# Kernel optimization log

Measured on AMD Instinct MI355X. Metric: run time of the kernel, lower is better.

The kernel has to match this reference:

```python
import jax, jax.numpy as jnp
import numpy as np

N = 100000
E = 3200000
C = 40
L_CORR = 10
L_SMOOTH = 10
ALPHA_CORR = 0.979
ALPHA_SMOOTH = 0.756


def setup_inputs() -> dict:
    key = jax.random.key(0)
    k1, k2, k3, k4 = jax.random.split(key, 4)
    y_true = jax.random.randint(k1, (N,), 0, C, dtype=jnp.int32)
    y_soft = jax.random.uniform(k2, (N, C), dtype=jnp.float32)
    y_soft = y_soft / y_soft.sum(axis=1, keepdims=True)
    spread_mask = jax.random.randint(k3, (N,), 0, 2, dtype=jnp.int32).astype(bool)
    edge_index = jax.random.randint(k4, (2, E), 0, N, dtype=jnp.int32)
    return {"y_true": y_true, "y_soft": y_soft, "spread_mask": spread_mask,
            "edge_index": edge_index}


def _gcn_norm(src, dst, n):
    # symmetric normalization D^-1/2 A D^-1/2 from the edge list
    deg = jax.ops.segment_sum(jnp.ones_like(dst, dtype=jnp.float32), dst,
                              num_segments=n)
    dinv = jnp.where(deg > 0, jax.lax.rsqrt(jnp.maximum(deg, 1.0)), 0.0)
    return dinv[src] * dinv[dst]  # [E]


def _label_prop(y0, src, dst, norm, n, alpha, n_layers, post_step):
    # out <- post_step(alpha * A_hat @ out + (1 - alpha) * y0), repeated
    def body(_, out):
        agg = jax.ops.segment_sum(out[src] * norm[:, None], dst,
                                  num_segments=n)  # [N, C]
        return post_step(alpha * agg + (1.0 - alpha) * y0)
    return jax.lax.fori_loop(0, n_layers, body, y0)


def _correct_and_smooth(y_true, y_soft, spread_mask, edge_index):
    src, dst = edge_index[0], edge_index[1]
    norm = _gcn_norm(src, dst, N)
    onehot = jax.nn.one_hot(y_true, C, dtype=y_soft.dtype)  # [N, C]
    m = spread_mask[:, None]

    # ---- correct: propagate masked residual error, autoscale path ----
    error = jnp.where(m, onehot - y_soft, 0.0)
    smoothed_error = _label_prop(error, src, dst, norm, N, ALPHA_CORR,
                                 L_CORR, lambda x: jnp.clip(x, -1.0, 1.0))
    numel = jnp.sum(spread_mask).astype(y_soft.dtype)
    sigma = jnp.sum(jnp.abs(error)) / numel  # error is zero off-mask
    denom = jnp.sum(jnp.abs(smoothed_error), axis=1, keepdims=True)
    scale = sigma / denom  # [N, 1]
    scale = jnp.where(jnp.isinf(scale) | (scale > 1000.0), 1.0, scale)
    y_corr = y_soft + scale * smoothed_error

    # ---- smooth: inject true labels on spread_mask, propagate w/ softmax ----
    y0 = jnp.where(m, onehot, y_corr)
    out = _label_prop(y0, src, dst, norm, N, ALPHA_SMOOTH, L_SMOOTH,
                      lambda x: jax.nn.softmax(x, axis=-1))
    return out


def reference(y_true, y_soft, spread_mask, edge_index):
    return _correct_and_smooth(y_true, y_soft, spread_mask, edge_index)
```

## Files before the change

kernel.cpp:

```cpp
#include <hip/hip_runtime.h>
#include <hip/hip_fp16.h>
#include <math.h>

#define C 40

__global__ void k_detect(const unsigned int* __restrict__ w, int nwords,
                         unsigned int* __restrict__ flags) {
    int i = blockIdx.x * blockDim.x + threadIdx.x;
    unsigned int viol = 0;
    for (; i < nwords; i += gridDim.x * blockDim.x) {
        unsigned int v = w[i];
        if (!(v == 0u || v == 1u)) viol |= 1u;
        if (!(v == 0u || v == 0x3F800000u)) viol |= 2u;
    }
    if (viol) atomicOr(flags, viol);
}

__device__ __forceinline__ bool read_mask(const void* mp, unsigned int fl, int n) {
    if ((fl & 1u) == 0u) return ((const int*)mp)[n] != 0;
    if ((fl & 2u) == 0u) return ((const float*)mp)[n] != 0.0f;
    return ((const unsigned char*)mp)[n] != 0;
}

__global__ void k_slot(const int* __restrict__ dst, int* __restrict__ fill,
                       int* __restrict__ slots, int E) {
    int e = blockIdx.x * blockDim.x + threadIdx.x;
    if (e < E) slots[e] = atomicAdd(&fill[dst[e]], 1);
}

__global__ void k_dinv(const int* __restrict__ deg, float* __restrict__ dinv, int n) {
    int i = blockIdx.x * blockDim.x + threadIdx.x;
    if (i < n) {
        int d = deg[i];
        dinv[i] = (d > 0) ? rsqrtf((float)d) : 0.0f;
    }
}

__global__ void k_scan1(const int* __restrict__ in, int* __restrict__ outp,
                        int* __restrict__ bsum, int n) {
    __shared__ int sm[256];
    int tid = threadIdx.x;
    int i = blockIdx.x * 256 + tid;
    int v = (i < n) ? in[i] : 0;
    sm[tid] = v;
    __syncthreads();
#pragma unroll
    for (int o = 1; o < 256; o <<= 1) {
        int t = (tid >= o) ? sm[tid - o] : 0;
        __syncthreads();
        sm[tid] += t;
        __syncthreads();
    }
    if (i <= n) outp[i] = sm[tid] - v;
    if (tid == 255) bsum[blockIdx.x] = sm[255];
}

__global__ void k_scan2(int* __restrict__ bsum, int nb) {
    __shared__ int sm[512];
    int tid = threadIdx.x;
    int v = (tid < nb) ? bsum[tid] : 0;
    sm[tid] = v;
    __syncthreads();
    for (int o = 1; o < 512; o <<= 1) {
        int t = (tid >= o) ? sm[tid - o] : 0;
        __syncthreads();
        sm[tid] += t;
        __syncthreads();
    }
    if (tid < nb) bsum[tid] = sm[tid] - v;
}

__global__ void k_scan3(int* __restrict__ outp, const int* __restrict__ bsum, int n) {
    int i = blockIdx.x * 256 + threadIdx.x;
    if (i <= n) outp[i] += bsum[blockIdx.x];
}

__global__ void k_wr(const int* __restrict__ src, const int* __restrict__ dst,
                     const int* __restrict__ slots, const float* __restrict__ dinv,
                     const int* __restrict__ rowptr,
                     unsigned long long* __restrict__ pk, int E) {
    int e = blockIdx.x * blockDim.x + threadIdx.x;
    if (e < E) {
        int d = dst[e], s = src[e];
        int pos = rowptr[d] + slots[e];
        unsigned long long u = (unsigned)s |
            ((unsigned long long)(unsigned)__float_as_int(dinv[s] * dinv[d]) << 32);
        pk[pos] = u;
    }
}

__global__ __launch_bounds__(256) void k_error(
    const float4* __restrict__ ys4, const int* __restrict__ y_true,
    const void* __restrict__ maskp, const unsigned int* __restrict__ flags,
    char* __restrict__ err, float* __restrict__ psig, float* __restrict__ pcnt,
    int n) {
    unsigned int fl = *flags;
    unsigned boff = (unsigned)n * 64u;
    float a = 0.f, cnt = 0.f;
    int nq = n * 10;
    for (int i = blockIdx.x * blockDim.x + threadIdx.x; i < nq;
         i += gridDim.x * blockDim.x) {
        int node = i / 10;
        int q = i - node * 10;
        float e0 = 0.f, e1 = 0.f, e2 = 0.f, e3 = 0.f;
        if (read_mask(maskp, fl, node)) {
            int yt = y_true[node];
            float4 ys = ys4[i];
            int c0 = q * 4;
            e0 = ((c0 + 0) == yt ? 1.f : 0.f) - ys.x;
            e1 = ((c0 + 1) == yt ? 1.f : 0.f) - ys.y;
            e2 = ((c0 + 2) == yt ? 1.f : 0.f) - ys.z;
            e3 = ((c0 + 3) == yt ? 1.f : 0.f) - ys.w;
            a += fabsf(e0) + fabsf(e1) + fabsf(e2) + fabsf(e3);
            if (q == 0) cnt += 1.f;
        }
        __half2 h01 = __floats2half2_rn(e0, e1);
        __half2 h23 = __floats2half2_rn(e2, e3);
        uint2 w;
        w.x = *(unsigned*)&h01;
        w.y = *(unsigned*)&h23;
        unsigned off = (q < 8) ? (unsigned)node * 64u + (unsigned)q * 8u
                               : boff + (unsigned)node * 16u + (unsigned)(q - 8) * 8u;
        *(uint2*)(err + off) = w;
    }
    __shared__ float sA[256];
    __shared__ float sB[256];
    int tid = threadIdx.x;
    sA[tid] = a; sB[tid] = cnt;
    __syncthreads();
    for (int o = 128; o; o >>= 1) {
        if (tid < o) { sA[tid] += sA[tid + o]; sB[tid] += sB[tid + o]; }
        __syncthreads();
    }
    if (tid == 0) { psig[blockIdx.x] = sA[0]; pcnt[blockIdx.x] = sB[0]; }
}

__global__ __launch_bounds__(256) void k_reduce(
    const float* __restrict__ psig, const float* __restrict__ pcnt,
    float* __restrict__ s_sig, float* __restrict__ s_cnt, int nb) {
    float a = 0.f, c = 0.f;
    for (int i = threadIdx.x; i < nb; i += 256) { a += psig[i]; c += pcnt[i]; }
    __shared__ float sA[256];
    __shared__ float sB[256];
    int tid = threadIdx.x;
    sA[tid] = a; sB[tid] = c;
    __syncthreads();
    for (int o = 128; o; o >>= 1) {
        if (tid < o) { sA[tid] += sA[tid + o]; sB[tid] += sB[tid + o]; }
        __syncthreads();
    }
    if (tid == 0) { *s_sig = sA[0]; *s_cnt = sB[0]; }
}

template <int POST, int F32OUT>
__global__ __launch_bounds__(256, 2) void k_prop(
    const int* __restrict__ rowptr, const unsigned long long* __restrict__ pk8,
    const char* __restrict__ xc, const char* __restrict__ y0,
    void* __restrict__ outv, float alpha, float beta, int n) {
    int wid = (blockIdx.x * blockDim.x + threadIdx.x) >> 6;
    int lane = threadIdx.x & 63;
    if (wid >= n) return;
    int beg = __builtin_amdgcn_readfirstlane(rowptr[wid]);
    int end = __builtin_amdgcn_readfirstlane(rowptr[wid + 1]);
    int deg = end - beg;
    int j = lane / 10;
    int k = lane - j * 10;
    unsigned shift = (k < 8) ? 6u : 4u;
    unsigned off = (k < 8) ? (unsigned)(k * 8)
                           : (unsigned)n * 64u + (unsigned)((k - 8) * 8);

    uint2 yv = *(const uint2*)(y0 + (((unsigned)wid << shift) + off));
    __half2 yh01 = *(__half2*)&yv.x;
    __half2 yh23 = *(__half2*)&yv.y;
    float2 yf01 = __half22float2(yh01);
    float2 yf23 = __half22float2(yh23);

    float a0 = 0.f, a1 = 0.f, a2 = 0.f, a3 = 0.f;

    unsigned s_[8];
    float n_[8];
    int dm1 = (deg > 0) ? deg - 1 : 0;
#pragma unroll
    for (int i = 0; i < 8; ++i) {
        int idx = j + 6 * i;
        int cl = idx < dm1 ? idx : dm1;
        unsigned long long u = pk8[beg + cl];
        s_[i] = (unsigned)(u & 0xffffffffu);
        bool val = (lane < 60) && (idx < deg);
        n_[i] = val ? __int_as_float((int)(u >> 32)) : 0.0f;
    }
    uint2 xv[8];
#pragma unroll
    for (int i = 0; i < 8; ++i)
        xv[i] = *(const uint2*)(xc + (((unsigned)s_[i] << shift) + off));
#pragma unroll
    for (int i = 0; i < 8; ++i) {
        __half2 h01 = *(__half2*)&xv[i].x;
        __half2 h23 = *(__half2*)&xv[i].y;
        float2 f01 = __half22float2(h01);
        float2 f23 = __half22float2(h23);
        a0 = fmaf(n_[i], f01.x, a0); a1 = fmaf(n_[i], f01.y, a1);
        a2 = fmaf(n_[i], f23.x, a2); a3 = fmaf(n_[i], f23.y, a3);
    }

    int rem = deg - 48;
    if (rem > 0) {
        int jbig = (lane < 60) ? j : 0x40000000;
        unsigned jo = (unsigned)(((lane < 60) ? j : 5) * 8);
        const char* pkc = (const char*)(pk8 + beg);
        int t = 48;
        for (; rem > 0; rem -= 12, t += 12) {
            unsigned long long ua = *(const unsigned long long*)(pkc + (size_t)t * 8 + jo);
            unsigned long long ub = *(const unsigned long long*)(pkc + (size_t)(t + 6) * 8 + jo);
            unsigned sa = (unsigned)(ua & 0xffffffffu);
            unsigned sb = (unsigned)(ub & 0xffffffffu);
            uint2 xa = *(const uint2*)(xc + ((sa << shift) + off));
            uint2 xb = *(const uint2*)(xc + ((sb << shift) + off));
            float na = (jbig < rem) ? __int_as_float((int)(ua >> 32)) : 0.0f;
            float nb = (jbig < rem - 6) ? __int_as_float((int)(ub >> 32)) : 0.0f;
            __half2 ha01 = *(__half2*)&xa.x;
            __half2 ha23 = *(__half2*)&xa.y;
            float2 fa01 = __half22float2(ha01);
            float2 fa23 = __half22float2(ha23);
            a0 = fmaf(na, fa01.x, a0); a1 = fmaf(na, fa01.y, a1);
            a2 = fmaf(na, fa23.x, a2); a3 = fmaf(na, fa23.y, a3);
            __half2 hb01 = *(__half2*)&xb.x;
            __half2 hb23 = *(__half2*)&xb.y;
            float2 fb01 = __half22float2(hb01);
            float2 fb23 = __half22float2(hb23);
            a0 = fmaf(nb, fb01.x, a0); a1 = fmaf(nb, fb01.y, a1);
            a2 = fmaf(nb, fb23.x, a2); a3 = fmaf(nb, fb23.y, a3);
        }
    }

    a0 += __shfl(a0, lane + 30); a1 += __shfl(a1, lane + 30);
    a2 += __shfl(a2, lane + 30); a3 += __shfl(a3, lane + 30);
    float t0a = __shfl(a0, lane + 10), t1a = __shfl(a1, lane + 10);
    float t2a = __shfl(a2, lane + 10), t3a = __shfl(a3, lane + 10);
    float t0b = __shfl(a0, lane + 20), t1b = __shfl(a1, lane + 20);
    float t2b = __shfl(a2, lane + 20), t3b = __shfl(a3, lane + 20);
    a0 += t0a + t0b; a1 += t1a + t1b; a2 += t2a + t2b; a3 += t3a + t3b;

    float v0 = fmaf(alpha, a0, beta * yf01.x);
    float v1 = fmaf(alpha, a1, beta * yf01.y);
    float v2 = fmaf(alpha, a2, beta * yf23.x);
    float v3 = fmaf(alpha, a3, beta * yf23.y);

    bool valid = (lane < 10);
    float r0, r1, r2, r3;
    if (POST == 0) {
        r0 = fminf(1.0f, fmaxf(-1.0f, v0));
        r1 = fminf(1.0f, fmaxf(-1.0f, v1));
        r2 = fminf(1.0f, fmaxf(-1.0f, v2));
        r3 = fminf(1.0f, fmaxf(-1.0f, v3));
    } else {
        float mx = valid ? fmaxf(fmaxf(v0, v1), fmaxf(v2, v3)) : -3.0e38f;
#pragma unroll
        for (int o = 8; o; o >>= 1) mx = fmaxf(mx, __shfl_xor(mx, o));
        float e0 = valid ? __expf(v0 - mx) : 0.f;
        float e1 = valid ? __expf(v1 - mx) : 0.f;
        float e2 = valid ? __expf(v2 - mx) : 0.f;
        float e3 = valid ? __expf(v3 - mx) : 0.f;
        float ss = (e0 + e1) + (e2 + e3);
#pragma unroll
        for (int o = 8; o; o >>= 1) ss += __shfl_xor(ss, o);
        float inv = 1.0f / ss;
        r0 = e0 * inv; r1 = e1 * inv; r2 = e2 * inv; r3 = e3 * inv;
    }

    if (valid) {
        if (F32OUT) {
            ((float4*)outv)[(size_t)wid * 10 + k] = make_float4(r0, r1, r2, r3);
        } else {
            __half2 h01 = __floats2half2_rn(r0, r1);
            __half2 h23 = __floats2half2_rn(r2, r3);
            uint2 w;
            w.x = *(unsigned*)&h01;
            w.y = *(unsigned*)&h23;
            *(uint2*)((char*)outv + (((unsigned)wid << shift) + off)) = w;
        }
    }
}

__global__ __launch_bounds__(256) void k_scale(
    const char* __restrict__ sm_err, const float* __restrict__ y_soft,
    const int* __restrict__ y_true, const void* __restrict__ maskp,
    const unsigned int* __restrict__ flags, const float* __restrict__ s_sig,
    const float* __restrict__ s_cnt, char* __restrict__ y0, int n) {
    int wid = (blockIdx.x * blockDim.x + threadIdx.x) >> 6;
    int lane = threadIdx.x & 63;
    if (wid >= n) return;
    bool isA = (lane < 32);
    unsigned shift = isA ? 6u : 4u;
    unsigned aoff = isA ? (unsigned)(lane * 2)
                        : (unsigned)n * 64u + (unsigned)((lane - 32) * 2);
    float v = 0.f, a = 0.f;
    if (lane < C) {
        v = __half2float(*(const __half*)(sm_err + (((unsigned)wid << shift) + aoff)));
        a = fabsf(v);
    }
#pragma unroll
    for (int o = 32; o; o >>= 1) a += __shfl_xor(a, o);
    float sigma = (*s_sig) / (*s_cnt);
    float scale = sigma / a;
    if (isinf(scale) || scale > 1000.0f) scale = 1.0f;
    if (lane < C) {
        bool m = read_mask(maskp, *flags, wid);
        float yc = fmaf(scale, v, y_soft[(size_t)wid * C + lane]);
        float r = m ? ((lane == y_true[wid]) ? 1.0f : 0.0f) : yc;
        *(__half*)(y0 + (((unsigned)wid << shift) + aoff)) = __float2half(r);
    }
}

extern "C" void kernel_launch(void* const* d_in, const int* in_sizes, int n_in,
                              void* d_out, int out_size, void* d_ws, size_t ws_size,
                              hipStream_t stream) {
    const int* y_true = (const int*)d_in[0];
    const float* y_soft = (const float*)d_in[1];
    const void* maskp = d_in[2];
    const int* ei = (const int*)d_in[3];
    const int n = in_sizes[0];
    const int E = in_sizes[3] / 2;
    const int* src = ei;
    const int* dst = ei + E;

    char* ws = (char*)d_ws;
    size_t off = 0;
    auto alloc = [&](size_t bytes) -> char* {
        char* p = ws + off;
        off += (bytes + 255) & ~(size_t)255;
        return p;
    };
    int* fill = (int*)alloc((size_t)n * 4);
    unsigned int* flags = (unsigned int*)alloc(4);
    size_t zero_bytes = off;
    float* s_sig = (float*)alloc(4);
    float* s_cnt = (float*)alloc(4);
    float* psig = (float*)alloc(2048 * 4);
    float* pcnt = (float*)alloc(2048 * 4);
    float* dinv = (float*)alloc((size_t)n * 4);
    int* rowptr = (int*)alloc((size_t)(n + 1) * 4);
    int* bsum = (int*)alloc(4096);
    int* slots = (int*)alloc((size_t)E * 4);
    unsigned long long* pk = (unsigned long long*)alloc(((size_t)E + 64) * 8);
    size_t fb = (size_t)n * 80 + 512;
    char* hE = alloc(fb);
    char* hY = alloc(fb);
    char* hA = alloc(fb);
    char* hB = alloc(fb);
    (void)ws_size;

    hipMemsetAsync(d_ws, 0, zero_bytes, stream);
    hipMemsetAsync(pk + E, 0, 64 * 8, stream);

    k_detect<<<98, 256, 0, stream>>>((const unsigned int*)maskp, n / 4, flags);
    k_slot<<<(E + 255) / 256, 256, 0, stream>>>(dst, fill, slots, E);
    k_dinv<<<(n + 255) / 256, 256, 0, stream>>>(fill, dinv, n);

    int nb1 = (n + 1 + 255) / 256;
    k_scan1<<<nb1, 256, 0, stream>>>(fill, rowptr, bsum, n);
    k_scan2<<<1, 512, 0, stream>>>(bsum, nb1);
    k_scan3<<<nb1, 256, 0, stream>>>(rowptr, bsum, n);
    k_wr<<<(E + 255) / 256, 256, 0, stream>>>(src, dst, slots, dinv, rowptr, pk, E);

    k_error<<<2048, 256, 0, stream>>>((const float4*)y_soft, y_true, maskp, flags,
                                      hE, psig, pcnt, n);
    k_reduce<<<1, 256, 0, stream>>>(psig, pcnt, s_sig, s_cnt, 2048);

    const int pb = (n + 3) / 4;
    const float A1 = 0.979f, B1 = (float)(1.0 - 0.979);
    const float A2 = 0.756f, B2 = (float)(1.0 - 0.756);
    char* bufs[2] = { hA, hB };

    const char* x = hE;
    for (int it = 0; it < 10; ++it) {
        k_prop<0, 0><<<pb, 256, 0, stream>>>(rowptr, pk, x, hE, bufs[it & 1], A1, B1, n);
        x = bufs[it & 1];
    }
    k_scale<<<pb, 256, 0, stream>>>(x, y_soft, y_true, maskp, flags, s_sig, s_cnt, hY, n);

    x = hY;
    for (int it = 0; it < 9; ++it) {
        k_prop<1, 0><<<pb, 256, 0, stream>>>(rowptr, pk, x, hY, bufs[it & 1], A2, B2, n);
        x = bufs[it & 1];
    }
    k_prop<1, 1><<<pb, 256, 0, stream>>>(rowptr, pk, x, hY, d_out, A2, B2, n);
}
```

Baseline: 1.458 ms.

## Split propagation into two source-range passes to shrink gather working set

```diff
diff --git a/kernel.cpp b/kernel.cpp
--- a/kernel.cpp
+++ b/kernel.cpp
@@ -22,16 +22,20 @@
     return ((const unsigned char*)mp)[n] != 0;
 }
 
-__global__ void k_slot(const int* __restrict__ dst, int* __restrict__ fill,
-                       int* __restrict__ slots, int E) {
+__global__ void k_slot(const int* __restrict__ src, const int* __restrict__ dst,
+                       int* __restrict__ fill, int* __restrict__ slots,
+                       int E, int half, int n) {
     int e = blockIdx.x * blockDim.x + threadIdx.x;
-    if (e < E) slots[e] = atomicAdd(&fill[dst[e]], 1);
-}
-
-__global__ void k_dinv(const int* __restrict__ deg, float* __restrict__ dinv, int n) {
+    if (e < E) {
+        int h = (src[e] >= half) ? n : 0;
+        slots[e] = atomicAdd(&fill[h + dst[e]], 1);
+    }
+}
+
+__global__ void k_dinv(const int* __restrict__ fill, float* __restrict__ dinv, int n) {
     int i = blockIdx.x * blockDim.x + threadIdx.x;
     if (i < n) {
-        int d = deg[i];
+        int d = fill[i] + fill[n + i];
         dinv[i] = (d > 0) ? rsqrtf((float)d) : 0.0f;
     }
 }
@@ -58,16 +62,31 @@
 __global__ void k_scan2(int* __restrict__ bsum, int nb) {
     __shared__ int sm[512];
     int tid = threadIdx.x;
-    int v = (tid < nb) ? bsum[tid] : 0;
-    sm[tid] = v;
+    int K = (nb + 511) / 512;
+    if (K > 8) K = 8;
+    int base = tid * K;
+    int loc[8];
+    int s = 0;
+    for (int i = 0; i < K; ++i) {
+        int idx = base + i;
+        int v = (idx < nb) ? bsum[idx] : 0;
+        loc[i] = s;
+        s += v;
+    }
+    sm[tid] = s;
     __syncthreads();
+    int v = s;
     for (int o = 1; o < 512; o <<= 1) {
         int t = (tid >= o) ? sm[tid - o] : 0;
         __syncthreads();
         sm[tid] += t;
         __syncthreads();
     }
-    if (tid < nb) bsum[tid] = sm[tid] - v;
+    int pre = sm[tid] - v;
+    for (int i = 0; i < K; ++i) {
+        int idx = base + i;
+        if (idx < nb) bsum[idx] = pre + loc[i];
+    }
 }
 
 __global__ void k_scan3(int* __restrict__ outp, const int* __restrict__ bsum, int n) {
@@ -77,12 +96,13 @@
 
 __global__ void k_wr(const int* __restrict__ src, const int* __restrict__ dst,
                      const int* __restrict__ slots, const float* __restrict__ dinv,
-                     const int* __restrict__ rowptr,
-                     unsigned long long* __restrict__ pk, int E) {
+                     const int* __restrict__ rowptrAll,
+                     unsigned long long* __restrict__ pk, int E, int half, int n) {
     int e = blockIdx.x * blockDim.x + threadIdx.x;
     if (e < E) {
         int d = dst[e], s = src[e];
-        int pos = rowptr[d] + slots[e];
+        int h = (s >= half) ? n : 0;
+        int pos = rowptrAll[h + d] + slots[e];
         unsigned long long u = (unsigned)s |
             ((unsigned long long)(unsigned)__float_as_int(dinv[s] * dinv[d]) << 32);
         pk[pos] = u;
@@ -152,11 +172,12 @@
     if (tid == 0) { *s_sig = sA[0]; *s_cnt = sB[0]; }
 }
 
-template <int POST, int F32OUT>
+template <int POST, int F32OUT, int PASS>
 __global__ __launch_bounds__(256, 2) void k_prop(
     const int* __restrict__ rowptr, const unsigned long long* __restrict__ pk8,
     const char* __restrict__ xc, const char* __restrict__ y0,
-    void* __restrict__ outv, float alpha, float beta, int n) {
+    float4* __restrict__ tmp, void* __restrict__ outv,
+    float alpha, float beta, int n) {
     int wid = (blockIdx.x * blockDim.x + threadIdx.x) >> 6;
     int lane = threadIdx.x & 63;
     if (wid >= n) return;
@@ -169,32 +190,26 @@
     unsigned off = (k < 8) ? (unsigned)(k * 8)
                            : (unsigned)n * 64u + (unsigned)((k - 8) * 8);
 
-    uint2 yv = *(const uint2*)(y0 + (((unsigned)wid << shift) + off));
-    __half2 yh01 = *(__half2*)&yv.x;
-    __half2 yh23 = *(__half2*)&yv.y;
-    float2 yf01 = __half22float2(yh01);
-    float2 yf23 = __half22float2(yh23);
-
     float a0 = 0.f, a1 = 0.f, a2 = 0.f, a3 = 0.f;
 
-    unsigned s_[8];
-    float n_[8];
+    unsigned s_[4];
+    float n_[4];
     int dm1 = (deg > 0) ? deg - 1 : 0;
 #pragma unroll
-    for (int i = 0; i < 8; ++i) {
+    for (int i = 0; i < 4; ++i) {
         int idx = j + 6 * i;
         int cl = idx < dm1 ? idx : dm1;
-        unsigned long long u = pk8[beg + cl];
+        unsigned long long u = __builtin_nontemporal_load(pk8 + beg + cl);
         s_[i] = (unsigned)(u & 0xffffffffu);
         bool val = (lane < 60) && (idx < deg);
         n_[i] = val ? __int_as_float((int)(u >> 32)) : 0.0f;
     }
-    uint2 xv[8];
-#pragma unroll
-    for (int i = 0; i < 8; ++i)
+    uint2 xv[4];
+#pragma unroll
+    for (int i = 0; i < 4; ++i)
         xv[i] = *(const uint2*)(xc + (((unsigned)s_[i] << shift) + off));
 #pragma unroll
-    for (int i = 0; i < 8; ++i) {
+    for (int i = 0; i < 4; ++i) {
         __half2 h01 = *(__half2*)&xv[i].x;
         __half2 h23 = *(__half2*)&xv[i].y;
         float2 f01 = __half22float2(h01);
@@ -203,12 +218,12 @@
         a2 = fmaf(n_[i], f23.x, a2); a3 = fmaf(n_[i], f23.y, a3);
     }
 
-    int rem = deg - 48;
+    int rem = deg - 24;
     if (rem > 0) {
         int jbig = (lane < 60) ? j : 0x40000000;
         unsigned jo = (unsigned)(((lane < 60) ? j : 5) * 8);
         const char* pkc = (const char*)(pk8 + beg);
-        int t = 48;
+        int t = 24;
         for (; rem > 0; rem -= 12, t += 12) {
             unsigned long long ua = *(const unsigned long long*)(pkc + (size_t)t * 8 + jo);
             unsigned long long ub = *(const unsigned long long*)(pkc + (size_t)(t + 6) * 8 + jo);
@@ -241,12 +256,38 @@
     float t2b = __shfl(a2, lane + 20), t3b = __shfl(a3, lane + 20);
     a0 += t0a + t0b; a1 += t1a + t1b; a2 += t2a + t2b; a3 += t3a + t3b;
 
+    bool valid = (lane < 10);
+
+    if (PASS == 0) {
+        if (valid) {
+            float2 lo = make_float2(a0, a1), hi = make_float2(a2, a3);
+            unsigned long long* p = (unsigned long long*)&tmp[(size_t)wid * 10 + k];
+            __builtin_nontemporal_store(*(unsigned long long*)&lo, p);
+            __builtin_nontemporal_store(*(unsigned long long*)&hi, p + 1);
+        }
+        return;
+    }
+
+    {
+        const unsigned long long* p =
+            (const unsigned long long*)&tmp[(size_t)wid * 10 + k];
+        unsigned long long u0 = __builtin_nontemporal_load(p);
+        unsigned long long u1 = __builtin_nontemporal_load(p + 1);
+        float2 lo = *(float2*)&u0, hi = *(float2*)&u1;
+        a0 += lo.x; a1 += lo.y; a2 += hi.x; a3 += hi.y;
+    }
+
+    uint2 yv = *(const uint2*)(y0 + (((unsigned)wid << shift) + off));
+    __half2 yh01 = *(__half2*)&yv.x;
+    __half2 yh23 = *(__half2*)&yv.y;
+    float2 yf01 = __half22float2(yh01);
+    float2 yf23 = __half22float2(yh23);
+
     float v0 = fmaf(alpha, a0, beta * yf01.x);
     float v1 = fmaf(alpha, a1, beta * yf01.y);
     float v2 = fmaf(alpha, a2, beta * yf23.x);
     float v3 = fmaf(alpha, a3, beta * yf23.y);
 
-    bool valid = (lane < 10);
     float r0, r1, r2, r3;
     if (POST == 0) {
         r0 = fminf(1.0f, fmaxf(-1.0f, v0));
@@ -323,6 +364,8 @@
     const int E = in_sizes[3] / 2;
     const int* src = ei;
     const int* dst = ei + E;
+    const int half = n / 2;
+    const int N2 = 2 * n;
 
     char* ws = (char*)d_ws;
     size_t off = 0;
@@ -331,7 +374,7 @@
         off += (bytes + 255) & ~(size_t)255;
         return p;
     };
-    int* fill = (int*)alloc((size_t)n * 4);
+    int* fill = (int*)alloc((size_t)N2 * 4);
     unsigned int* flags = (unsigned int*)alloc(4);
     size_t zero_bytes = off;
     float* s_sig = (float*)alloc(4);
@@ -339,10 +382,11 @@
     float* psig = (float*)alloc(2048 * 4);
     float* pcnt = (float*)alloc(2048 * 4);
     float* dinv = (float*)alloc((size_t)n * 4);
-    int* rowptr = (int*)alloc((size_t)(n + 1) * 4);
-    int* bsum = (int*)alloc(4096);
+    int* rowptrAll = (int*)alloc((size_t)(N2 + 1) * 4);
+    int* bsum = (int*)alloc(4096 * 4);
     int* slots = (int*)alloc((size_t)E * 4);
     unsigned long long* pk = (unsigned long long*)alloc(((size_t)E + 64) * 8);
+    float4* tmp = (float4*)alloc((size_t)n * 10 * 16);
     size_t fb = (size_t)n * 80 + 512;
     char* hE = alloc(fb);
     char* hY = alloc(fb);
@@ -354,14 +398,15 @@
     hipMemsetAsync(pk + E, 0, 64 * 8, stream);
 
     k_detect<<<98, 256, 0, stream>>>((const unsigned int*)maskp, n / 4, flags);
-    k_slot<<<(E + 255) / 256, 256, 0, stream>>>(dst, fill, slots, E);
+    k_slot<<<(E + 255) / 256, 256, 0, stream>>>(src, dst, fill, slots, E, half, n);
     k_dinv<<<(n + 255) / 256, 256, 0, stream>>>(fill, dinv, n);
 
-    int nb1 = (n + 1 + 255) / 256;
-    k_scan1<<<nb1, 256, 0, stream>>>(fill, rowptr, bsum, n);
+    int nb1 = (N2 + 1 + 255) / 256;
+    k_scan1<<<nb1, 256, 0, stream>>>(fill, rowptrAll, bsum, N2);
     k_scan2<<<1, 512, 0, stream>>>(bsum, nb1);
-    k_scan3<<<nb1, 256, 0, stream>>>(rowptr, bsum, n);
-    k_wr<<<(E + 255) / 256, 256, 0, stream>>>(src, dst, slots, dinv, rowptr, pk, E);
+    k_scan3<<<nb1, 256, 0, stream>>>(rowptrAll, bsum, N2);
+    k_wr<<<(E + 255) / 256, 256, 0, stream>>>(src, dst, slots, dinv, rowptrAll,
+                                              pk, E, half, n);
 
     k_error<<<2048, 256, 0, stream>>>((const float4*)y_soft, y_true, maskp, flags,
                                       hE, psig, pcnt, n);
@@ -374,15 +419,24 @@
 
     const char* x = hE;
     for (int it = 0; it < 10; ++it) {
-        k_prop<0, 0><<<pb, 256, 0, stream>>>(rowptr, pk, x, hE, bufs[it & 1], A1, B1, n);
+        k_prop<0, 0, 0><<<pb, 256, 0, stream>>>(rowptrAll, pk, x, hE, tmp,
+                                                bufs[it & 1], A1, B1, n);
+        k_prop<0, 0, 1><<<pb, 256, 0, stream>>>(rowptrAll + n, pk, x, hE, tmp,
+                                                bufs[it & 1], A1, B1, n);
         x = bufs[it & 1];
     }
     k_scale<<<pb, 256, 0, stream>>>(x, y_soft, y_true, maskp, flags, s_sig, s_cnt, hY, n);
 
     x = hY;
     for (int it = 0; it < 9; ++it) {
-        k_prop<1, 0><<<pb, 256, 0, stream>>>(rowptr, pk, x, hY, bufs[it & 1], A2, B2, n);
+        k_prop<1, 0, 0><<<pb, 256, 0, stream>>>(rowptrAll, pk, x, hY, tmp,
+                                                bufs[it & 1], A2, B2, n);
+        k_prop<1, 0, 1><<<pb, 256, 0, stream>>>(rowptrAll + n, pk, x, hY, tmp,
+                                                bufs[it & 1], A2, B2, n);
         x = bufs[it & 1];
     }
-    k_prop<1, 1><<<pb, 256, 0, stream>>>(rowptr, pk, x, hY, d_out, A2, B2, n);
-}
+    k_prop<1, 1, 0><<<pb, 256, 0, stream>>>(rowptrAll, pk, x, hY, tmp,
+                                            d_out, A2, B2, n);
+    k_prop<1, 1, 1><<<pb, 256, 0, stream>>>(rowptrAll + n, pk, x, hY, tmp,
+                                            d_out, A2, B2, n);
+}
```

After: 1.995 ms. 36.8% more time.

## Privatize degree-count atomics per XCD to avoid cross-die atomic traffic

Applied to the files above, without the earlier changes.

```diff
diff --git a/kernel.cpp b/kernel.cpp
--- a/kernel.cpp
+++ b/kernel.cpp
@@ -22,10 +22,28 @@
     return ((const unsigned char*)mp)[n] != 0;
 }
 
-__global__ void k_slot(const int* __restrict__ dst, int* __restrict__ fill,
-                       int* __restrict__ slots, int E) {
+__global__ void k_slot(const int* __restrict__ dst, int* __restrict__ fillx,
+                       int* __restrict__ slots, int E, int n) {
     int e = blockIdx.x * blockDim.x + threadIdx.x;
-    if (e < E) slots[e] = atomicAdd(&fill[dst[e]], 1);
+    unsigned xcd = __builtin_amdgcn_s_getreg(6164) & 7u;
+    if (e < E) {
+        int r = atomicAdd(&fillx[xcd * (unsigned)n + (unsigned)dst[e]], 1);
+        slots[e] = (int)((xcd << 28) | (unsigned)r);
+    }
+}
+
+__global__ void k_off(int* __restrict__ fillx, int* __restrict__ deg, int n) {
+    int i = blockIdx.x * blockDim.x + threadIdx.x;
+    if (i < n) {
+        int s = 0;
+#pragma unroll
+        for (int x = 0; x < 8; ++x) {
+            int v = fillx[x * n + i];
+            fillx[x * n + i] = s;
+            s += v;
+        }
+        deg[i] = s;
+    }
 }
 
 __global__ void k_dinv(const int* __restrict__ deg, float* __restrict__ dinv, int n) {
@@ -76,13 +94,16 @@
 }
 
 __global__ void k_wr(const int* __restrict__ src, const int* __restrict__ dst,
-                     const int* __restrict__ slots, const float* __restrict__ dinv,
-                     const int* __restrict__ rowptr,
-                     unsigned long long* __restrict__ pk, int E) {
+                     const int* __restrict__ slots, const int* __restrict__ fillx,
+                     const float* __restrict__ dinv, const int* __restrict__ rowptr,
+                     unsigned long long* __restrict__ pk, int E, int n) {
     int e = blockIdx.x * blockDim.x + threadIdx.x;
     if (e < E) {
         int d = dst[e], s = src[e];
-        int pos = rowptr[d] + slots[e];
+        unsigned sl = (unsigned)slots[e];
+        unsigned xcd = sl >> 28;
+        int r = (int)(sl & 0x0fffffffu);
+        int pos = rowptr[d] + fillx[xcd * (unsigned)n + (unsigned)d] + r;
         unsigned long long u = (unsigned)s |
             ((unsigned long long)(unsigned)__float_as_int(dinv[s] * dinv[d]) << 32);
         pk[pos] = u;
@@ -331,9 +352,10 @@
         off += (bytes + 255) & ~(size_t)255;
         return p;
     };
-    int* fill = (int*)alloc((size_t)n * 4);
+    int* fillx = (int*)alloc((size_t)n * 8 * 4);
     unsigned int* flags = (unsigned int*)alloc(4);
     size_t zero_bytes = off;
+    int* deg = (int*)alloc((size_t)n * 4);
     float* s_sig = (float*)alloc(4);
     float* s_cnt = (float*)alloc(4);
     float* psig = (float*)alloc(2048 * 4);
@@ -354,14 +376,16 @@
     hipMemsetAsync(pk + E, 0, 64 * 8, stream);
 
     k_detect<<<98, 256, 0, stream>>>((const unsigned int*)maskp, n / 4, flags);
-    k_slot<<<(E + 255) / 256, 256, 0, stream>>>(dst, fill, slots, E);
-    k_dinv<<<(n + 255) / 256, 256, 0, stream>>>(fill, dinv, n);
+    k_slot<<<(E + 255) / 256, 256, 0, stream>>>(dst, fillx, slots, E, n);
+    k_off<<<(n + 255) / 256, 256, 0, stream>>>(fillx, deg, n);
+    k_dinv<<<(n + 255) / 256, 256, 0, stream>>>(deg, dinv, n);
 
     int nb1 = (n + 1 + 255) / 256;
-    k_scan1<<<nb1, 256, 0, stream>>>(fill, rowptr, bsum, n);
+    k_scan1<<<nb1, 256, 0, stream>>>(deg, rowptr, bsum, n);
     k_scan2<<<1, 512, 0, stream>>>(bsum, nb1);
     k_scan3<<<nb1, 256, 0, stream>>>(rowptr, bsum, n);
-    k_wr<<<(E + 255) / 256, 256, 0, stream>>>(src, dst, slots, dinv, rowptr, pk, E);
+    k_wr<<<(E + 255) / 256, 256, 0, stream>>>(src, dst, slots, fillx, dinv,
+                                              rowptr, pk, E, n);
 
     k_error<<<2048, 256, 0, stream>>>((const float4*)y_soft, y_true, maskp, flags,
                                       hE, psig, pcnt, n);
```

Result: no change. 1.466 ms (+0.6%).
